# Kernel optimization log

Hardware: AMD Instinct MI355X
Metric: run time of the kernel (lower is better)

The kernel has to match this reference:

```python
import jax, jax.numpy as jnp
import numpy as np

EMBED_DIM = 1024
Q_HEADS = 8
KV_HEADS = 4
HEAD_DIM = EMBED_DIM // Q_HEADS          # 128
KV_EMBED_DIM = HEAD_DIM * KV_HEADS       # 512
LN_EPS = 1e-5
RMS_EPS = 1e-6


def _activation_quant(x):
    # per-token int8 quant over last dim
    scale = 127.0 / jnp.clip(jnp.max(jnp.abs(x), axis=-1, keepdims=True), 1e-5)
    return jnp.clip(jnp.round(x * scale), -128, 127) / scale


def _weight_quant(w):
    # ternary (sign) quant with global mean-abs scale
    scale = jnp.mean(jnp.abs(w))
    e = jnp.mean(w)
    return jnp.sign(w - e) * scale


def bit_linear(x, w):
    # fresh RMSNorm with weight=ones (as in the torch code: RMSNorm(d)(x))
    x_norm = x * jax.lax.rsqrt(jnp.mean(x * x, axis=-1, keepdims=True) + RMS_EPS)
    # straight-through estimators
    x_q = x_norm + jax.lax.stop_gradient(_activation_quant(x_norm) - x_norm)
    w_q = w + jax.lax.stop_gradient(_weight_quant(w) - w)
    # F.linear(x_quant, w_quant): NO bias (the torch forward ignores self.bias)
    return jnp.einsum('bnd,od->bno', x_q, w_q)


def setup_inputs() -> dict:
    key = jax.random.key(0)
    ks = jax.random.split(key, 7)
    B, S = 4, 2048

    def xavier(k, shape):
        std = (2.0 / (shape[0] + shape[1])) ** 0.5
        return std * jax.random.normal(k, shape, dtype=jnp.float32)

    return {
        'query': jax.random.normal(ks[0], (B, S, EMBED_DIM), dtype=jnp.float32),
        'key':   jax.random.normal(ks[1], (B, S, EMBED_DIM), dtype=jnp.float32),
        'value': jax.random.normal(ks[2], (B, S, EMBED_DIM), dtype=jnp.float32),
        'q_w':   xavier(ks[3], (EMBED_DIM, EMBED_DIM)),
        'k_w':   xavier(ks[4], (KV_EMBED_DIM, EMBED_DIM)),
        'v_w':   xavier(ks[5], (KV_EMBED_DIM, EMBED_DIM)),
        'out_w': xavier(ks[6], (EMBED_DIM, KV_EMBED_DIM)),
        'ln_gamma': jnp.ones((KV_EMBED_DIM,), dtype=jnp.float32),
        'ln_beta':  jnp.zeros((KV_EMBED_DIM,), dtype=jnp.float32),
    }


def reference(query, key, value, q_w, k_w, v_w, out_w, ln_gamma, ln_beta):
    B, N, _ = query.shape
    q = bit_linear(query, q_w)   # [b, n, embed_dim]
    k = bit_linear(key,   k_w)   # [b, s, kv_embed_dim]
    v = bit_linear(value, v_w)   # [b, s, kv_embed_dim]

    g = Q_HEADS // KV_HEADS  # head groups
    # b n (hq d) -> b hq n d -> b hk g n d  (head index = h*g + g_idx, matching
    # einops 'b (h g) n d -> b g h n d')
    q = q.reshape(B, N, Q_HEADS, HEAD_DIM).transpose(0, 2, 1, 3)
    q = q.reshape(B, KV_HEADS, g, N, HEAD_DIM)
    k = k.reshape(B, -1, KV_HEADS, HEAD_DIM).transpose(0, 2, 1, 3)  # b h s d
    v = v.reshape(B, -1, KV_HEADS, HEAD_DIM).transpose(0, 2, 1, 3)  # b h s d

    scale = HEAD_DIM ** 0.5
    q = q / scale
    # note: the original SUMS over the group axis g (faithful to einops einsum)
    sim = jnp.einsum('bhgnd,bhsd->bhns', q, k)
    # note: original divides by scale AGAIN before softmax
    attn = jax.nn.softmax(sim / scale, axis=-1)
    out = jnp.einsum('bhns,bhsd->bnhd', attn, v)        # b n hk d
    x = out.reshape(B, N, KV_EMBED_DIM)

    # LayerNorm over kv_embed_dim
    mu = jnp.mean(x, axis=-1, keepdims=True)
    var = jnp.mean((x - mu) ** 2, axis=-1, keepdims=True)
    x = (x - mu) * jax.lax.rsqrt(var + LN_EPS) * ln_gamma + ln_beta

    return bit_linear(x, out_w)  # [b, n, embed_dim]
```

## Files before the change

kernel.cpp:

```cpp
#include <hip/hip_runtime.h>
#include <cstdint>
#include <cstddef>

constexpr int B_   = 4;
constexpr int SEQ  = 2048;
constexpr int E    = 1024;
constexpr int KVE  = 512;
constexpr int H    = 4;
constexpr int ROWS = B_ * SEQ;

typedef short short8   __attribute__((ext_vector_type(8)));
typedef short short4v  __attribute__((ext_vector_type(4)));
typedef float floatx4  __attribute__((ext_vector_type(4)));
typedef float floatx16 __attribute__((ext_vector_type(16)));
typedef int   intx4    __attribute__((ext_vector_type(4)));

__device__ inline short f2bf(float f) {
    uint32_t u = __builtin_bit_cast(uint32_t, f);
    u = (u + 0x7fff + ((u >> 16) & 1)) >> 16;
    return (short)u;
}
__device__ inline float bf2f(short s) {
    return __builtin_bit_cast(float, (uint32_t)(uint16_t)s << 16);
}
__device__ inline void gl_lds16(const void* g, void* l) {
    __builtin_amdgcn_global_load_lds(
        (const __attribute__((address_space(1))) unsigned int*)g,
        (__attribute__((address_space(3))) unsigned int*)l, 16, 0, 0);
}

__global__ __launch_bounds__(256) void wstats_kernel(
    const float* __restrict__ w0, const float* __restrict__ w1,
    const float* __restrict__ w2, const float* __restrict__ w3,
    int n0, int n1, int n2, int n3, float* __restrict__ stats)
{
    int m = blockIdx.y;
    const float* w = (m == 0) ? w0 : (m == 1) ? w1 : (m == 2) ? w2 : w3;
    int n = (m == 0) ? n0 : (m == 1) ? n1 : (m == 2) ? n2 : n3;
    float s = 0.f, sa = 0.f;
    for (int i = blockIdx.x * 256 + threadIdx.x; i < n; i += gridDim.x * 256) {
        float x = w[i];
        s += x; sa += fabsf(x);
    }
#pragma unroll
    for (int o = 32; o; o >>= 1) { s += __shfl_xor(s, o); sa += __shfl_xor(sa, o); }
    __shared__ float ls[4], lsa[4];
    int lane = threadIdx.x & 63, wv = threadIdx.x >> 6;
    if (!lane) { ls[wv] = s; lsa[wv] = sa; }
    __syncthreads();
    if (!threadIdx.x) {
        atomicAdd(&stats[2 * m],     ls[0] + ls[1] + ls[2] + ls[3]);
        atomicAdd(&stats[2 * m + 1], lsa[0] + lsa[1] + lsa[2] + lsa[3]);
    }
}

__global__ __launch_bounds__(256) void wquant_kernel(
    const float* __restrict__ w0, const float* __restrict__ w1,
    const float* __restrict__ w2, const float* __restrict__ w3,
    int n0, int n1, int n2, int n3, const float* __restrict__ stats,
    int8_t* __restrict__ o0, int8_t* __restrict__ o1,
    int8_t* __restrict__ o2, int8_t* __restrict__ o3)
{
    int m = blockIdx.y;
    const float* w = (m == 0) ? w0 : (m == 1) ? w1 : (m == 2) ? w2 : w3;
    int n = (m == 0) ? n0 : (m == 1) ? n1 : (m == 2) ? n2 : n3;
    int8_t* o = (m == 0) ? o0 : (m == 1) ? o1 : (m == 2) ? o2 : o3;
    float e = stats[2 * m] / (float)n;
    int n4 = n >> 2;
    for (int i = blockIdx.x * 256 + threadIdx.x; i < n4; i += gridDim.x * 256) {
        float4 x = ((const float4*)w)[i];
        int q0 = (x.x > e) - (x.x < e);
        int q1 = (x.y > e) - (x.y < e);
        int q2 = (x.z > e) - (x.z < e);
        int q3 = (x.w > e) - (x.w < e);
        uint32_t pk = (uint32_t)(q0 & 0xff) | ((uint32_t)(q1 & 0xff) << 8) |
                      ((uint32_t)(q2 & 0xff) << 16) | ((uint32_t)(q3 & 0xff) << 24);
        *(uint32_t*)(o + ((size_t)i << 2)) = pk;
    }
}

__global__ __launch_bounds__(256) void aquant3_kernel(
    const float* __restrict__ q, const float* __restrict__ k,
    const float* __restrict__ vv, int8_t* __restrict__ xq01,
    int8_t* __restrict__ xq2, float* __restrict__ dqv)
{
    int lane = threadIdx.x & 63, wv = threadIdx.x >> 6;
    int rowi = blockIdx.x * 4 + wv;
    int z = rowi >> 13, r = rowi & (ROWS - 1);
    const float* x = (z == 0) ? q : (z == 1) ? k : vv;
    int8_t* xq = (z == 2) ? xq2 : xq01 + (size_t)z * ROWS * E;
    size_t base = (size_t)r * E;
    float4 v[4];
    float ss = 0.f, am = 0.f;
#pragma unroll
    for (int j = 0; j < 4; j++) {
        v[j] = *(const float4*)(x + base + lane * 4 + j * 256);
        ss += v[j].x * v[j].x + v[j].y * v[j].y + v[j].z * v[j].z + v[j].w * v[j].w;
        am = fmaxf(am, fmaxf(fmaxf(fabsf(v[j].x), fabsf(v[j].y)),
                             fmaxf(fabsf(v[j].z), fabsf(v[j].w))));
    }
#pragma unroll
    for (int o = 32; o; o >>= 1) { ss += __shfl_xor(ss, o); am = fmaxf(am, __shfl_xor(am, o)); }
    float rms = rsqrtf(ss * (1.0f / E) + 1e-6f);
    float cl  = fmaxf(am * rms, 1e-5f);
    float kf  = rms * (127.0f / cl);
#pragma unroll
    for (int j = 0; j < 4; j++) {
        int q0 = max(-128, min(127, (int)rintf(v[j].x * kf)));
        int q1 = max(-128, min(127, (int)rintf(v[j].y * kf)));
        int q2 = max(-128, min(127, (int)rintf(v[j].z * kf)));
        int q3 = max(-128, min(127, (int)rintf(v[j].w * kf)));
        uint32_t pk = (uint32_t)(q0 & 0xff) | ((uint32_t)(q1 & 0xff) << 8) |
                      ((uint32_t)(q2 & 0xff) << 16) | ((uint32_t)(q3 & 0xff) << 24);
        *(uint32_t*)(xq + base + lane * 4 + j * 256) = pk;
    }
    if (!lane) dqv[(size_t)z * ROWS + r] = cl * (1.0f / 127.0f);
}

template <bool F32OUT>
__device__ inline void gemm_body(
    const int8_t* __restrict__ A, const int8_t* __restrict__ W,
    const float* __restrict__ dqv, float sw, void* __restrict__ Cout,
    int O, int K, int8_t* As, int8_t* Ws, size_t row0, size_t c0)
{
    int tid = threadIdx.x;
    int w = tid >> 6, lane = tid & 63;
    int quad = lane >> 4, l15 = lane & 15;
    int mbase = (w & 1) * 64, nbase = (w >> 1) * 64;

    intx4 acc[4][4];
#pragma unroll
    for (int i = 0; i < 4; i++)
#pragma unroll
        for (int j = 0; j < 4; j++) acc[i][j] = (intx4){0, 0, 0, 0};

    int cA0 = tid, cA1 = tid + 256;
    int rA0 = cA0 >> 2, gA0 = (cA0 & 3) ^ (rA0 & 3);
    int rA1 = cA1 >> 2, gA1 = (cA1 & 3) ^ (rA1 & 3);
    const int8_t* Ag0 = A + (row0 + rA0) * K + gA0 * 16;
    const int8_t* Ag1 = A + (row0 + rA1) * K + gA1 * 16;
    const int8_t* Wg0 = W + (c0 + rA0) * K + gA0 * 16;
    const int8_t* Wg1 = W + (c0 + rA1) * K + gA1 * 16;
    int8_t* lA0 = As + cA0 * 16;  int8_t* lA1 = As + cA1 * 16;
    int8_t* lW0 = Ws + cA0 * 16;  int8_t* lW1 = Ws + cA1 * 16;

    for (int kt = 0; kt < K; kt += 64) {
        __syncthreads();
        gl_lds16(Ag0 + kt, lA0);
        gl_lds16(Ag1 + kt, lA1);
        gl_lds16(Wg0 + kt, lW0);
        gl_lds16(Wg1 + kt, lW1);
        __syncthreads();
        intx4 af[4], bfr[4];
#pragma unroll
        for (int mt = 0; mt < 4; mt++) {
            int row = mbase + mt * 16 + l15;
            int pos = quad ^ (row & 3);
            af[mt] = *(const intx4*)(As + row * 64 + pos * 16);
        }
#pragma unroll
        for (int nt = 0; nt < 4; nt++) {
            int row = nbase + nt * 16 + l15;
            int pos = quad ^ (row & 3);
            bfr[nt] = *(const intx4*)(Ws + row * 64 + pos * 16);
        }
#pragma unroll
        for (int mt = 0; mt < 4; mt++)
#pragma unroll
            for (int nt = 0; nt < 4; nt++)
                acc[mt][nt] = __builtin_amdgcn_mfma_i32_16x16x64_i8(
                    af[mt], bfr[nt], acc[mt][nt], 0, 0, 0);
    }

#pragma unroll
    for (int mt = 0; mt < 4; mt++) {
#pragma unroll
        for (int r = 0; r < 4; r++) {
            size_t grow = row0 + mbase + mt * 16 + quad * 4 + r;
            float scv = sw * dqv[grow];
#pragma unroll
            for (int nt = 0; nt < 4; nt++) {
                size_t gcol = c0 + nbase + nt * 16 + l15;
                float v = (float)acc[mt][nt][r] * scv;
                if constexpr (F32OUT) ((float*)Cout)[grow * O + gcol] = v;
                else                  ((short*)Cout)[grow * O + gcol] = f2bf(v);
            }
        }
    }
}

__global__ __launch_bounds__(256) void gemm_qkv(
    const int8_t* __restrict__ xq01, const int8_t* __restrict__ xq2,
    const int8_t* __restrict__ wq_q, const int8_t* __restrict__ wq_k,
    const int8_t* __restrict__ wq_v, const float* __restrict__ dqv,
    const float* __restrict__ stats,
    short* __restrict__ qb, short* __restrict__ kb, short* __restrict__ vb)
{
    __shared__ int8_t As[128 * 64];
    __shared__ int8_t Ws[128 * 64];
    int id = blockIdx.x;
    int z, bx, by;
    if (id < 512)      { z = 0; bx = id & 7; by = id >> 3; }
    else if (id < 768) { z = 1; int t = id - 512; bx = t & 3; by = t >> 2; }
    else               { z = 2; int t = id - 768; bx = t & 3; by = t >> 2; }
    int O = z ? KVE : E;
    const int8_t* A = (z == 0) ? xq01 : (z == 1) ? xq01 + (size_t)ROWS * E : xq2;
    const int8_t* W = (z == 0) ? wq_q : (z == 1) ? wq_k : wq_v;
    short* outp = (z == 0) ? qb : (z == 1) ? kb : vb;
    float sw = stats[2 * z + 1] / (float)(O * E);
    gemm_body<false>(A, W, dqv + (size_t)z * ROWS, sw, outp, O, E, As, Ws,
                     (size_t)by * 128, (size_t)bx * 128);
}

__global__ __launch_bounds__(256) void gemm_out(
    const int8_t* __restrict__ A, const int8_t* __restrict__ W,
    const float* __restrict__ dqv, const float* __restrict__ stats,
    float* __restrict__ Cout)
{
    __shared__ int8_t As[128 * 64];
    __shared__ int8_t Ws[128 * 64];
    float sw = stats[7] / (float)(E * KVE);
    gemm_body<true>(A, W, dqv, sw, Cout, E, KVE, As, Ws,
                    (size_t)blockIdx.y * 128, (size_t)blockIdx.x * 128);
}

__global__ __launch_bounds__(256, 2) void attn_mfma(
    const short* __restrict__ qb, const short* __restrict__ kb,
    const short* __restrict__ vb, float* __restrict__ opart,
    float* __restrict__ mlbuf)
{
    __shared__ short Ks[64][132];
    __shared__ short Vt[128][68];
    __shared__ short Ps[128][68];
    int tid = threadIdx.x;
    int w = tid >> 6, lane = tid & 63;
    int l31 = lane & 31, hi = lane >> 5;
    int blk = blockIdx.x, h = blockIdx.y, half = blockIdx.z;
    int b = blk >> 4;
    size_t qrow0 = (size_t)blk * 128;
    size_t sbase = (size_t)b * SEQ + (size_t)half * (SEQ / 2);

    int sK = tid >> 2, cK = tid & 3;
    int sV = (tid & 15) * 4, dV = tid >> 4;

    short8 kreg[4], vreg[4];
    {
        const short* ksrc = kb + (sbase + sK) * KVE + h * 128 + cK * 32;
#pragma unroll
        for (int j = 0; j < 4; j++) kreg[j] = *(const short8*)(ksrc + j * 8);
        const short* vsrc = vb + (sbase + sV) * KVE + h * 128 + dV * 8;
#pragma unroll
        for (int j = 0; j < 4; j++) vreg[j] = *(const short8*)(vsrc + j * KVE);
    }

    short8 qfrag[8];
    {
        const short* src = qb + (qrow0 + w * 32 + l31) * E + h * 256 + hi * 8;
#pragma unroll
        for (int j = 0; j < 8; j++) {
            short8 a  = *(const short8*)(src + j * 16);
            short8 b2 = *(const short8*)(src + j * 16 + 128);
            short8 o;
#pragma unroll
            for (int e = 0; e < 8; e++)
                o[e] = f2bf((bf2f(a[e]) + bf2f(b2[e])) * (1.0f / 128.0f));
            qfrag[j] = o;
        }
    }

    floatx16 oacc[4];
#pragma unroll
    for (int dt = 0; dt < 4; dt++)
#pragma unroll
        for (int r = 0; r < 16; r++) oacc[dt][r] = 0.f;
    float m_s = -1e30f, l_s = 0.f;

    for (int st = 0; st < SEQ / 128; st++) {
        __syncthreads();
#pragma unroll
        for (int j = 0; j < 4; j++)
            *(short8*)&Ks[sK][cK * 32 + j * 8] = kreg[j];
#pragma unroll
        for (int i = 0; i < 8; i++) {
            short4v vv = { vreg[0][i], vreg[1][i], vreg[2][i], vreg[3][i] };
            *(short4v*)&Vt[dV * 8 + i][sV] = vv;
        }
        if (st + 1 < SEQ / 128) {
            size_t srow0 = sbase + (size_t)(st + 1) * 64;
            const short* ksrc = kb + (srow0 + sK) * KVE + h * 128 + cK * 32;
#pragma unroll
            for (int j = 0; j < 4; j++) kreg[j] = *(const short8*)(ksrc + j * 8);
            const short* vsrc = vb + (srow0 + sV) * KVE + h * 128 + dV * 8;
#pragma unroll
            for (int j = 0; j < 4; j++) vreg[j] = *(const short8*)(vsrc + j * KVE);
        }
        __syncthreads();
        floatx16 sc0, sc1;
#pragma unroll
        for (int r = 0; r < 16; r++) { sc0[r] = 0.f; sc1[r] = 0.f; }
#pragma unroll
        for (int j = 0; j < 8; j++) {
            short8 kf0 = *(const short8*)&Ks[l31][j * 16 + hi * 8];
            short8 kf1 = *(const short8*)&Ks[32 + l31][j * 16 + hi * 8];
            sc0 = __builtin_amdgcn_mfma_f32_32x32x16_bf16(kf0, qfrag[j], sc0, 0, 0, 0);
            sc1 = __builtin_amdgcn_mfma_f32_32x32x16_bf16(kf1, qfrag[j], sc1, 0, 0, 0);
        }
        float mx = sc0[0];
#pragma unroll
        for (int r = 0; r < 16; r++) { mx = fmaxf(mx, sc0[r]); mx = fmaxf(mx, sc1[r]); }
        mx = fmaxf(mx, __shfl_xor(mx, 32));
        float nm = fmaxf(m_s, mx);
        float alpha = __expf(m_s - nm);
        m_s = nm;
        float rs = 0.f;
#pragma unroll
        for (int r = 0; r < 16; r++) {
            float p0 = __expf(sc0[r] - nm); sc0[r] = p0; rs += p0;
            float p1 = __expf(sc1[r] - nm); sc1[r] = p1; rs += p1;
        }
        rs += __shfl_xor(rs, 32);
        l_s = l_s * alpha + rs;
        int qrow = w * 32 + l31;
#pragma unroll
        for (int c = 0; c < 4; c++) {
            short4v p0 = { f2bf(sc0[c * 4]), f2bf(sc0[c * 4 + 1]),
                           f2bf(sc0[c * 4 + 2]), f2bf(sc0[c * 4 + 3]) };
            *(short4v*)&Ps[qrow][c * 8 + hi * 4] = p0;
            short4v p1 = { f2bf(sc1[c * 4]), f2bf(sc1[c * 4 + 1]),
                           f2bf(sc1[c * 4 + 2]), f2bf(sc1[c * 4 + 3]) };
            *(short4v*)&Ps[qrow][32 + c * 8 + hi * 4] = p1;
        }
#pragma unroll
        for (int dt = 0; dt < 4; dt++)
#pragma unroll
            for (int r = 0; r < 16; r++) oacc[dt][r] *= alpha;
        short8 pb[4];
#pragma unroll
        for (int j = 0; j < 4; j++)
            pb[j] = *(const short8*)&Ps[qrow][j * 16 + hi * 8];
#pragma unroll
        for (int dt = 0; dt < 4; dt++)
#pragma unroll
            for (int j = 0; j < 4; j++) {
                short8 vf = *(const short8*)&Vt[dt * 32 + l31][j * 16 + hi * 8];
                oacc[dt] = __builtin_amdgcn_mfma_f32_32x32x16_bf16(vf, pb[j], oacc[dt], 0, 0, 0);
            }
    }
    {
        float inv = 1.0f / l_s;
        size_t grow = qrow0 + w * 32 + l31;
        float* dst = opart + ((size_t)half * ROWS + grow) * KVE + h * 128;
#pragma unroll
        for (int dt = 0; dt < 4; dt++)
#pragma unroll
            for (int c = 0; c < 4; c++) {
                float4 o4 = { oacc[dt][c * 4] * inv, oacc[dt][c * 4 + 1] * inv,
                              oacc[dt][c * 4 + 2] * inv, oacc[dt][c * 4 + 3] * inv };
                *(float4*)(dst + dt * 32 + c * 8 + hi * 4) = o4;
            }
        if (hi == 0) {
            float* ml = mlbuf + (((size_t)half * ROWS + grow) * H + h) * 2;
            ml[0] = m_s;
            ml[1] = l_s;
        }
    }
}

__global__ __launch_bounds__(256) void ln_combine_kernel(
    const float* __restrict__ opart, const float* __restrict__ mlbuf,
    const float* __restrict__ gamma, const float* __restrict__ beta,
    int8_t* __restrict__ xq, float* __restrict__ dqv)
{
    int lane = threadIdx.x & 63, wv = threadIdx.x >> 6;
    int row = blockIdx.x * 4 + wv;
    float4 y[2];
    float s = 0.f, ss = 0.f;
#pragma unroll
    for (int j = 0; j < 2; j++) {
        int col = lane * 4 + j * 256;
        int h = j * 2 + (lane >> 5);
        const float* ml0 = mlbuf + ((size_t)row * H + h) * 2;
        const float* ml1 = mlbuf + (((size_t)ROWS + row) * H + h) * 2;
        float m1 = ml0[0], l1v = ml0[1], m2 = ml1[0], l2v = ml1[1];
        float M = fmaxf(m1, m2);
        float w1 = l1v * __expf(m1 - M), w2 = l2v * __expf(m2 - M);
        float winv = 1.0f / (w1 + w2);
        w1 *= winv; w2 *= winv;
        float4 o1 = *(const float4*)(opart + (size_t)row * KVE + col);
        float4 o2 = *(const float4*)(opart + ((size_t)ROWS + row) * KVE + col);
        float4 vv = { o1.x * w1 + o2.x * w2, o1.y * w1 + o2.y * w2,
                      o1.z * w1 + o2.z * w2, o1.w * w1 + o2.w * w2 };
        y[j] = vv;
        s += vv.x + vv.y + vv.z + vv.w;
        ss += vv.x * vv.x + vv.y * vv.y + vv.z * vv.z + vv.w * vv.w;
    }
#pragma unroll
    for (int o = 32; o; o >>= 1) { s += __shfl_xor(s, o); ss += __shfl_xor(ss, o); }
    float mu = s * (1.0f / KVE);
    float var = fmaxf(ss * (1.0f / KVE) - mu * mu, 0.0f);
    float inv = rsqrtf(var + 1e-5f);
    float sy = 0.f, am = 0.f;
#pragma unroll
    for (int j = 0; j < 2; j++) {
        int col = lane * 4 + j * 256;
        float4 g = *(const float4*)(gamma + col);
        float4 be = *(const float4*)(beta + col);
        y[j].x = (y[j].x - mu) * inv * g.x + be.x;
        y[j].y = (y[j].y - mu) * inv * g.y + be.y;
        y[j].z = (y[j].z - mu) * inv * g.z + be.z;
        y[j].w = (y[j].w - mu) * inv * g.w + be.w;
        sy += y[j].x * y[j].x + y[j].y * y[j].y + y[j].z * y[j].z + y[j].w * y[j].w;
        am = fmaxf(am, fmaxf(fmaxf(fabsf(y[j].x), fabsf(y[j].y)),
                             fmaxf(fabsf(y[j].z), fabsf(y[j].w))));
    }
#pragma unroll
    for (int o = 32; o; o >>= 1) { sy += __shfl_xor(sy, o); am = fmaxf(am, __shfl_xor(am, o)); }
    float rms = rsqrtf(sy * (1.0f / KVE) + 1e-6f);
    float cl = fmaxf(am * rms, 1e-5f);
    float kf = rms * (127.0f / cl);
#pragma unroll
    for (int j = 0; j < 2; j++) {
        int col = lane * 4 + j * 256;
        int q0 = max(-128, min(127, (int)rintf(y[j].x * kf)));
        int q1 = max(-128, min(127, (int)rintf(y[j].y * kf)));
        int q2 = max(-128, min(127, (int)rintf(y[j].z * kf)));
        int q3 = max(-128, min(127, (int)rintf(y[j].w * kf)));
        uint32_t pk = (uint32_t)(q0 & 0xff) | ((uint32_t)(q1 & 0xff) << 8) |
                      ((uint32_t)(q2 & 0xff) << 16) | ((uint32_t)(q3 & 0xff) << 24);
        *(uint32_t*)(xq + (size_t)row * KVE + col) = pk;
    }
    if (!lane) dqv[row] = cl * (1.0f / 127.0f);
}

extern "C" void kernel_launch(void* const* d_in, const int* in_sizes, int n_in,
                              void* d_out, int out_size, void* d_ws, size_t ws_size,
                              hipStream_t stream)
{
    const float* query = (const float*)d_in[0];
    const float* key   = (const float*)d_in[1];
    const float* value = (const float*)d_in[2];
    const float* q_w   = (const float*)d_in[3];
    const float* k_w   = (const float*)d_in[4];
    const float* v_w   = (const float*)d_in[5];
    const float* out_w = (const float*)d_in[6];
    const float* ln_g  = (const float*)d_in[7];
    const float* ln_b  = (const float*)d_in[8];
    float* out = (float*)d_out;

    char* p = (char*)d_ws;
    float* stats = (float*)p;  p += 256;
    int8_t* wq_q = (int8_t*)p; p += (size_t)1024 * 1024;
    int8_t* wq_k = (int8_t*)p; p += (size_t)512 * 1024;
    int8_t* wq_v = (int8_t*)p; p += (size_t)512 * 1024;
    int8_t* wq_o = (int8_t*)p; p += (size_t)1024 * 512;
    int8_t* xq01 = (int8_t*)p; p += (size_t)2 * ROWS * E;
    float* dqv  = (float*)p;   p += (size_t)3 * ROWS * 4;
    short* qb   = (short*)p;   p += (size_t)ROWS * E * 2;
    short* kb   = (short*)p;   p += (size_t)ROWS * KVE * 2;
    short* vb   = (short*)p;   p += (size_t)ROWS * KVE * 2;
    float* opart = (float*)p;  p += (size_t)2 * ROWS * KVE * 4;
    float* mlbuf = (float*)p;  p += (size_t)2 * ROWS * H * 2 * 4;
    int8_t* xq2 = (int8_t*)opart;
    if ((size_t)(p - (char*)d_ws) > ws_size) return;

    dim3 blk(256);
    hipMemsetAsync(stats, 0, 256, stream);
    wstats_kernel<<<dim3(64, 4), blk, 0, stream>>>(q_w, k_w, v_w, out_w,
        1024 * 1024, 512 * 1024, 512 * 1024, 1024 * 512, stats);
    wquant_kernel<<<dim3(64, 4), blk, 0, stream>>>(q_w, k_w, v_w, out_w,
        1024 * 1024, 512 * 1024, 512 * 1024, 1024 * 512, stats, wq_q, wq_k, wq_v, wq_o);

    aquant3_kernel<<<dim3(3 * ROWS / 4), blk, 0, stream>>>(query, key, value,
        xq01, xq2, dqv);
    gemm_qkv<<<dim3(1024), blk, 0, stream>>>(xq01, xq2, wq_q, wq_k, wq_v,
        dqv, stats, qb, kb, vb);

    attn_mfma<<<dim3(ROWS / 128, H, 2), blk, 0, stream>>>(qb, kb, vb, opart, mlbuf);

    ln_combine_kernel<<<dim3(ROWS / 4), blk, 0, stream>>>(opart, mlbuf,
        ln_g, ln_b, xq01, dqv);
    gemm_out<<<dim3(8, 64), blk, 0, stream>>>(xq01, wq_o, dqv, stats, out);
}
```

Measured before the change: 299.5 us.

## Merge weight stats into activation quant, widen GEMM K-tile, store attention partials as bf16

Folds the weight mean/abs-sum reduction into the same launch as the per-row activation quantization, removing one kernel launch and letting the two run concurrently. The int8 GEMM K-tile doubles from 64 to 128, using an 8-way XOR swizzle, which halves the barrier and load rounds per output tile at the cost of twice the shared memory. Attention split-K partial outputs are written and read as bf16 instead of fp32, halving that intermediate traffic. The bf16 partials add rounding error before the LayerNorm and requantization.

```diff
diff --git a/kernel.cpp b/kernel.cpp
--- a/kernel.cpp
+++ b/kernel.cpp
@@ -29,29 +29,67 @@
         (__attribute__((address_space(3))) unsigned int*)l, 16, 0, 0);
 }
 
-__global__ __launch_bounds__(256) void wstats_kernel(
+__global__ __launch_bounds__(256) void pre_kernel(
+    const float* __restrict__ qx, const float* __restrict__ kx,
+    const float* __restrict__ vx,
     const float* __restrict__ w0, const float* __restrict__ w1,
     const float* __restrict__ w2, const float* __restrict__ w3,
-    int n0, int n1, int n2, int n3, float* __restrict__ stats)
-{
-    int m = blockIdx.y;
-    const float* w = (m == 0) ? w0 : (m == 1) ? w1 : (m == 2) ? w2 : w3;
-    int n = (m == 0) ? n0 : (m == 1) ? n1 : (m == 2) ? n2 : n3;
-    float s = 0.f, sa = 0.f;
-    for (int i = blockIdx.x * 256 + threadIdx.x; i < n; i += gridDim.x * 256) {
-        float x = w[i];
-        s += x; sa += fabsf(x);
-    }
-#pragma unroll
-    for (int o = 32; o; o >>= 1) { s += __shfl_xor(s, o); sa += __shfl_xor(sa, o); }
-    __shared__ float ls[4], lsa[4];
-    int lane = threadIdx.x & 63, wv = threadIdx.x >> 6;
-    if (!lane) { ls[wv] = s; lsa[wv] = sa; }
-    __syncthreads();
-    if (!threadIdx.x) {
-        atomicAdd(&stats[2 * m],     ls[0] + ls[1] + ls[2] + ls[3]);
-        atomicAdd(&stats[2 * m + 1], lsa[0] + lsa[1] + lsa[2] + lsa[3]);
-    }
+    int8_t* __restrict__ xq01, int8_t* __restrict__ xq2,
+    float* __restrict__ dqv, float* __restrict__ stats)
+{
+    int tid = threadIdx.x, bid = blockIdx.x;
+    int lane = tid & 63, wv = tid >> 6;
+    if (bid < 256) {
+        int m = bid >> 6;
+        const float* w = (m == 0) ? w0 : (m == 1) ? w1 : (m == 2) ? w2 : w3;
+        int n4 = ((m == 0) ? 1024 * 1024 : 512 * 1024) >> 2;
+        float s = 0.f, sa = 0.f;
+        for (int i = (bid & 63) * 256 + tid; i < n4; i += 64 * 256) {
+            float4 x = ((const float4*)w)[i];
+            s += x.x + x.y + x.z + x.w;
+            sa += fabsf(x.x) + fabsf(x.y) + fabsf(x.z) + fabsf(x.w);
+        }
+#pragma unroll
+        for (int o = 32; o; o >>= 1) { s += __shfl_xor(s, o); sa += __shfl_xor(sa, o); }
+        __shared__ float ls[4], lsa[4];
+        if (!lane) { ls[wv] = s; lsa[wv] = sa; }
+        __syncthreads();
+        if (!tid) {
+            atomicAdd(&stats[2 * m],     ls[0] + ls[1] + ls[2] + ls[3]);
+            atomicAdd(&stats[2 * m + 1], lsa[0] + lsa[1] + lsa[2] + lsa[3]);
+        }
+        return;
+    }
+    int rowi = (bid - 256) * 4 + wv;
+    int z = rowi >> 13, r = rowi & (ROWS - 1);
+    const float* x = (z == 0) ? qx : (z == 1) ? kx : vx;
+    int8_t* xq = (z == 2) ? xq2 : xq01 + (size_t)z * ROWS * E;
+    size_t base = (size_t)r * E;
+    float4 v[4];
+    float ss = 0.f, am = 0.f;
+#pragma unroll
+    for (int j = 0; j < 4; j++) {
+        v[j] = *(const float4*)(x + base + lane * 4 + j * 256);
+        ss += v[j].x * v[j].x + v[j].y * v[j].y + v[j].z * v[j].z + v[j].w * v[j].w;
+        am = fmaxf(am, fmaxf(fmaxf(fabsf(v[j].x), fabsf(v[j].y)),
+                             fmaxf(fabsf(v[j].z), fabsf(v[j].w))));
+    }
+#pragma unroll
+    for (int o = 32; o; o >>= 1) { ss += __shfl_xor(ss, o); am = fmaxf(am, __shfl_xor(am, o)); }
+    float rms = rsqrtf(ss * (1.0f / E) + 1e-6f);
+    float cl  = fmaxf(am * rms, 1e-5f);
+    float kf  = rms * (127.0f / cl);
+#pragma unroll
+    for (int j = 0; j < 4; j++) {
+        int q0 = max(-128, min(127, (int)rintf(v[j].x * kf)));
+        int q1 = max(-128, min(127, (int)rintf(v[j].y * kf)));
+        int q2 = max(-128, min(127, (int)rintf(v[j].z * kf)));
+        int q3 = max(-128, min(127, (int)rintf(v[j].w * kf)));
+        uint32_t pk = (uint32_t)(q0 & 0xff) | ((uint32_t)(q1 & 0xff) << 8) |
+                      ((uint32_t)(q2 & 0xff) << 16) | ((uint32_t)(q3 & 0xff) << 24);
+        *(uint32_t*)(xq + base + lane * 4 + j * 256) = pk;
+    }
+    if (!lane) dqv[(size_t)z * ROWS + r] = cl * (1.0f / 127.0f);
 }
 
 __global__ __launch_bounds__(256) void wquant_kernel(
@@ -79,44 +117,6 @@
     }
 }
 
-__global__ __launch_bounds__(256) void aquant3_kernel(
-    const float* __restrict__ q, const float* __restrict__ k,
-    const float* __restrict__ vv, int8_t* __restrict__ xq01,
-    int8_t* __restrict__ xq2, float* __restrict__ dqv)
-{
-    int lane = threadIdx.x & 63, wv = threadIdx.x >> 6;
-    int rowi = blockIdx.x * 4 + wv;
-    int z = rowi >> 13, r = rowi & (ROWS - 1);
-    const float* x = (z == 0) ? q : (z == 1) ? k : vv;
-    int8_t* xq = (z == 2) ? xq2 : xq01 + (size_t)z * ROWS * E;
-    size_t base = (size_t)r * E;
-    float4 v[4];
-    float ss = 0.f, am = 0.f;
-#pragma unroll
-    for (int j = 0; j < 4; j++) {
-        v[j] = *(const float4*)(x + base + lane * 4 + j * 256);
-        ss += v[j].x * v[j].x + v[j].y * v[j].y + v[j].z * v[j].z + v[j].w * v[j].w;
-        am = fmaxf(am, fmaxf(fmaxf(fabsf(v[j].x), fabsf(v[j].y)),
-                             fmaxf(fabsf(v[j].z), fabsf(v[j].w))));
-    }
-#pragma unroll
-    for (int o = 32; o; o >>= 1) { ss += __shfl_xor(ss, o); am = fmaxf(am, __shfl_xor(am, o)); }
-    float rms = rsqrtf(ss * (1.0f / E) + 1e-6f);
-    float cl  = fmaxf(am * rms, 1e-5f);
-    float kf  = rms * (127.0f / cl);
-#pragma unroll
-    for (int j = 0; j < 4; j++) {
-        int q0 = max(-128, min(127, (int)rintf(v[j].x * kf)));
-        int q1 = max(-128, min(127, (int)rintf(v[j].y * kf)));
-        int q2 = max(-128, min(127, (int)rintf(v[j].z * kf)));
-        int q3 = max(-128, min(127, (int)rintf(v[j].w * kf)));
-        uint32_t pk = (uint32_t)(q0 & 0xff) | ((uint32_t)(q1 & 0xff) << 8) |
-                      ((uint32_t)(q2 & 0xff) << 16) | ((uint32_t)(q3 & 0xff) << 24);
-        *(uint32_t*)(xq + base + lane * 4 + j * 256) = pk;
-    }
-    if (!lane) dqv[(size_t)z * ROWS + r] = cl * (1.0f / 127.0f);
-}
-
 template <bool F32OUT>
 __device__ inline void gemm_body(
     const int8_t* __restrict__ A, const int8_t* __restrict__ W,
@@ -134,42 +134,47 @@
 #pragma unroll
         for (int j = 0; j < 4; j++) acc[i][j] = (intx4){0, 0, 0, 0};
 
-    int cA0 = tid, cA1 = tid + 256;
-    int rA0 = cA0 >> 2, gA0 = (cA0 & 3) ^ (rA0 & 3);
-    int rA1 = cA1 >> 2, gA1 = (cA1 & 3) ^ (rA1 & 3);
-    const int8_t* Ag0 = A + (row0 + rA0) * K + gA0 * 16;
-    const int8_t* Ag1 = A + (row0 + rA1) * K + gA1 * 16;
-    const int8_t* Wg0 = W + (c0 + rA0) * K + gA0 * 16;
-    const int8_t* Wg1 = W + (c0 + rA1) * K + gA1 * 16;
-    int8_t* lA0 = As + cA0 * 16;  int8_t* lA1 = As + cA1 * 16;
-    int8_t* lW0 = Ws + cA0 * 16;  int8_t* lW1 = Ws + cA1 * 16;
-
-    for (int kt = 0; kt < K; kt += 64) {
+    const int8_t* Ag[4]; const int8_t* Wg[4]; int8_t* lA[4]; int8_t* lW[4];
+#pragma unroll
+    for (int t = 0; t < 4; t++) {
+        int c = tid + t * 256;
+        int row = c >> 3, g = (c & 7) ^ (row & 7);
+        Ag[t] = A + (row0 + row) * K + g * 16;
+        Wg[t] = W + (c0 + row) * K + g * 16;
+        lA[t] = As + c * 16;
+        lW[t] = Ws + c * 16;
+    }
+
+    for (int kt = 0; kt < K; kt += 128) {
         __syncthreads();
-        gl_lds16(Ag0 + kt, lA0);
-        gl_lds16(Ag1 + kt, lA1);
-        gl_lds16(Wg0 + kt, lW0);
-        gl_lds16(Wg1 + kt, lW1);
+#pragma unroll
+        for (int t = 0; t < 4; t++) {
+            gl_lds16(Ag[t] + kt, lA[t]);
+            gl_lds16(Wg[t] + kt, lW[t]);
+        }
         __syncthreads();
-        intx4 af[4], bfr[4];
-#pragma unroll
-        for (int mt = 0; mt < 4; mt++) {
-            int row = mbase + mt * 16 + l15;
-            int pos = quad ^ (row & 3);
-            af[mt] = *(const intx4*)(As + row * 64 + pos * 16);
-        }
-#pragma unroll
-        for (int nt = 0; nt < 4; nt++) {
-            int row = nbase + nt * 16 + l15;
-            int pos = quad ^ (row & 3);
-            bfr[nt] = *(const intx4*)(Ws + row * 64 + pos * 16);
-        }
-#pragma unroll
-        for (int mt = 0; mt < 4; mt++)
-#pragma unroll
-            for (int nt = 0; nt < 4; nt++)
-                acc[mt][nt] = __builtin_amdgcn_mfma_i32_16x16x64_i8(
-                    af[mt], bfr[nt], acc[mt][nt], 0, 0, 0);
+#pragma unroll
+        for (int kh = 0; kh < 2; kh++) {
+            intx4 af[4], bfr[4];
+#pragma unroll
+            for (int mt = 0; mt < 4; mt++) {
+                int row = mbase + mt * 16 + l15;
+                int pos = (quad + 4 * kh) ^ (row & 7);
+                af[mt] = *(const intx4*)(As + row * 128 + pos * 16);
+            }
+#pragma unroll
+            for (int nt = 0; nt < 4; nt++) {
+                int row = nbase + nt * 16 + l15;
+                int pos = (quad + 4 * kh) ^ (row & 7);
+                bfr[nt] = *(const intx4*)(Ws + row * 128 + pos * 16);
+            }
+#pragma unroll
+            for (int mt = 0; mt < 4; mt++)
+#pragma unroll
+                for (int nt = 0; nt < 4; nt++)
+                    acc[mt][nt] = __builtin_amdgcn_mfma_i32_16x16x64_i8(
+                        af[mt], bfr[nt], acc[mt][nt], 0, 0, 0);
+        }
     }
 
 #pragma unroll
@@ -196,8 +201,8 @@
     const float* __restrict__ stats,
     short* __restrict__ qb, short* __restrict__ kb, short* __restrict__ vb)
 {
-    __shared__ int8_t As[128 * 64];
-    __shared__ int8_t Ws[128 * 64];
+    __shared__ int8_t As[128 * 128];
+    __shared__ int8_t Ws[128 * 128];
     int id = blockIdx.x;
     int z, bx, by;
     if (id < 512)      { z = 0; bx = id & 7; by = id >> 3; }
@@ -217,8 +222,8 @@
     const float* __restrict__ dqv, const float* __restrict__ stats,
     float* __restrict__ Cout)
 {
-    __shared__ int8_t As[128 * 64];
-    __shared__ int8_t Ws[128 * 64];
+    __shared__ int8_t As[128 * 128];
+    __shared__ int8_t Ws[128 * 128];
     float sw = stats[7] / (float)(E * KVE);
     gemm_body<true>(A, W, dqv, sw, Cout, E, KVE, As, Ws,
                     (size_t)blockIdx.y * 128, (size_t)blockIdx.x * 128);
@@ -226,7 +231,7 @@
 
 __global__ __launch_bounds__(256, 2) void attn_mfma(
     const short* __restrict__ qb, const short* __restrict__ kb,
-    const short* __restrict__ vb, float* __restrict__ opart,
+    const short* __restrict__ vb, short* __restrict__ opart,
     float* __restrict__ mlbuf)
 {
     __shared__ short Ks[64][132];
@@ -349,14 +354,16 @@
     {
         float inv = 1.0f / l_s;
         size_t grow = qrow0 + w * 32 + l31;
-        float* dst = opart + ((size_t)half * ROWS + grow) * KVE + h * 128;
+        short* dst = opart + ((size_t)half * ROWS + grow) * KVE + h * 128;
 #pragma unroll
         for (int dt = 0; dt < 4; dt++)
 #pragma unroll
             for (int c = 0; c < 4; c++) {
-                float4 o4 = { oacc[dt][c * 4] * inv, oacc[dt][c * 4 + 1] * inv,
-                              oacc[dt][c * 4 + 2] * inv, oacc[dt][c * 4 + 3] * inv };
-                *(float4*)(dst + dt * 32 + c * 8 + hi * 4) = o4;
+                short4v o4 = { f2bf(oacc[dt][c * 4] * inv),
+                               f2bf(oacc[dt][c * 4 + 1] * inv),
+                               f2bf(oacc[dt][c * 4 + 2] * inv),
+                               f2bf(oacc[dt][c * 4 + 3] * inv) };
+                *(short4v*)(dst + dt * 32 + c * 8 + hi * 4) = o4;
             }
         if (hi == 0) {
             float* ml = mlbuf + (((size_t)half * ROWS + grow) * H + h) * 2;
@@ -367,7 +374,7 @@
 }
 
 __global__ __launch_bounds__(256) void ln_combine_kernel(
-    const float* __restrict__ opart, const float* __restrict__ mlbuf,
+    const short* __restrict__ opart, const float* __restrict__ mlbuf,
     const float* __restrict__ gamma, const float* __restrict__ beta,
     int8_t* __restrict__ xq, float* __restrict__ dqv)
 {
@@ -386,10 +393,12 @@
         float w1 = l1v * __expf(m1 - M), w2 = l2v * __expf(m2 - M);
         float winv = 1.0f / (w1 + w2);
         w1 *= winv; w2 *= winv;
-        float4 o1 = *(const float4*)(opart + (size_t)row * KVE + col);
-        float4 o2 = *(const float4*)(opart + ((size_t)ROWS + row) * KVE + col);
-        float4 vv = { o1.x * w1 + o2.x * w2, o1.y * w1 + o2.y * w2,
-                      o1.z * w1 + o2.z * w2, o1.w * w1 + o2.w * w2 };
+        short4v o1 = *(const short4v*)(opart + (size_t)row * KVE + col);
+        short4v o2 = *(const short4v*)(opart + ((size_t)ROWS + row) * KVE + col);
+        float4 vv = { bf2f(o1.x) * w1 + bf2f(o2.x) * w2,
+                      bf2f(o1.y) * w1 + bf2f(o2.y) * w2,
+                      bf2f(o1.z) * w1 + bf2f(o2.z) * w2,
+                      bf2f(o1.w) * w1 + bf2f(o2.w) * w2 };
         y[j] = vv;
         s += vv.x + vv.y + vv.z + vv.w;
         ss += vv.x * vv.x + vv.y * vv.y + vv.z * vv.z + vv.w * vv.w;
@@ -458,20 +467,18 @@
     short* qb   = (short*)p;   p += (size_t)ROWS * E * 2;
     short* kb   = (short*)p;   p += (size_t)ROWS * KVE * 2;
     short* vb   = (short*)p;   p += (size_t)ROWS * KVE * 2;
-    float* opart = (float*)p;  p += (size_t)2 * ROWS * KVE * 4;
+    short* opart = (short*)p;  p += (size_t)2 * ROWS * KVE * 2;
     float* mlbuf = (float*)p;  p += (size_t)2 * ROWS * H * 2 * 4;
     int8_t* xq2 = (int8_t*)opart;
     if ((size_t)(p - (char*)d_ws) > ws_size) return;
 
     dim3 blk(256);
     hipMemsetAsync(stats, 0, 256, stream);
-    wstats_kernel<<<dim3(64, 4), blk, 0, stream>>>(q_w, k_w, v_w, out_w,
-        1024 * 1024, 512 * 1024, 512 * 1024, 1024 * 512, stats);
+    pre_kernel<<<dim3(256 + 3 * ROWS / 4), blk, 0, stream>>>(query, key, value,
+        q_w, k_w, v_w, out_w, xq01, xq2, dqv, stats);
     wquant_kernel<<<dim3(64, 4), blk, 0, stream>>>(q_w, k_w, v_w, out_w,
         1024 * 1024, 512 * 1024, 512 * 1024, 1024 * 512, stats, wq_q, wq_k, wq_v, wq_o);
 
-    aquant3_kernel<<<dim3(3 * ROWS / 4), blk, 0, stream>>>(query, key, value,
-        xq01, xq2, dqv);
     gemm_qkv<<<dim3(1024), blk, 0, stream>>>(xq01, xq2, wq_q, wq_k, wq_v,
         dqv, stats, qb, kb, vb);
 
```

Result: faster. 266.6 us (-11.0%).
